# Optimization experiments

Hardware: AMD Instinct MI355X
Metric: run time of the kernel (lower is better)

The kernel has to match this reference:

```python
import jax, jax.numpy as jnp
import numpy as np

DIM = 768
HEADS = 12
HEAD_DIM = DIM // HEADS
SCALE = HEAD_DIM ** -0.5
EPS = 1e-6


def setup_inputs() -> dict:
    key = jax.random.key(0)
    ks = jax.random.split(key, 10)
    B, Nq, Nk, C = 4, 4096, 4096, DIM
    std = C ** -0.5
    return {
        "x_q": jax.random.normal(ks[0], (B, Nq, C), jnp.float32),
        "x_kv": jax.random.normal(ks[1], (B, Nk, C), jnp.float32),
        "Wq": jax.random.normal(ks[2], (C, C), jnp.float32) * std,
        "bq": jnp.zeros((C,), jnp.float32),
        "Wk": jax.random.normal(ks[3], (C, C), jnp.float32) * std,
        "bk": jnp.zeros((C,), jnp.float32),
        "Wv": jax.random.normal(ks[4], (C, C), jnp.float32) * std,
        "bv": jnp.zeros((C,), jnp.float32),
        "Wp": jax.random.normal(ks[5], (C, C), jnp.float32) * std,
        "bp": jnp.zeros((C,), jnp.float32),
    }


def _phi(x):
    # ELU(alpha=1) + 1 positive feature map
    return jax.nn.elu(x) + 1.0


def reference(x_q, x_kv, Wq, bq, Wk, bk, Wv, bv, Wp, bp):
    B, Nq, C = x_q.shape
    Nk = x_kv.shape[1]
    h, d = HEADS, HEAD_DIM
    # projections (torch Linear: x @ W.T + b)
    q = x_q @ Wq.T + bq   # [B,Nq,C]
    k = x_kv @ Wk.T + bk  # [B,Nk,C]
    v = x_kv @ Wv.T + bv  # [B,Nk,C]
    # split heads -> [B,h,N,d]
    q = q.reshape(B, Nq, h, d).transpose(0, 2, 1, 3) * SCALE
    k = k.reshape(B, Nk, h, d).transpose(0, 2, 1, 3)
    v = v.reshape(B, Nk, h, d).transpose(0, 2, 1, 3)
    q_phi = _phi(q)
    k_phi = _phi(k)
    # KV state [B,h,d,d] and normalizer sum [B,h,d]
    kv = jnp.einsum('bhnd,bhne->bhde', k_phi, v)
    k_sum = k_phi.sum(axis=2)
    out = jnp.einsum('bhnd,bhde->bhne', q_phi, kv)
    z = jnp.einsum('bhnd,bhd->bhn', q_phi, k_sum)[..., None] + EPS
    out = out / z
    out = out.transpose(0, 2, 1, 3).reshape(B, Nq, C)
    return out @ Wp.T + bp
```

## Files before the change

### kernel.cpp

```cpp
#include <hip/hip_runtime.h>
#include <hip/hip_bf16.h>
#include <cstdint>
#include <cstddef>

#define HD_B   4
#define SEQ    4096
#define CDIM   768
#define HEADS  12
#define HDIM   64
#define MROWS  (HD_B * SEQ)
#define QSCALE 0.125f
#define EPSV   1e-6f

typedef __attribute__((ext_vector_type(8))) short  short8v;
typedef __attribute__((ext_vector_type(4))) float  f32x4;

__device__ __forceinline__ unsigned short f2b(float f) {
    unsigned int u = __float_as_uint(f);
    u += 0x7FFFu + ((u >> 16) & 1u);
    return (unsigned short)(u >> 16);
}
__device__ __forceinline__ float b2f(unsigned short b) {
    return __uint_as_float(((unsigned int)b) << 16);
}
__device__ __forceinline__ float phi_f(float x) {
    return x > 0.f ? x + 1.f : __expf(x);
}

#define GLOAD_LDS16(g, l)                                             \
    __builtin_amdgcn_global_load_lds(                                 \
        (__attribute__((address_space(1))) void*)(void*)(g),          \
        (__attribute__((address_space(3))) void*)(l), 16, 0, 0)

#define VMW12() asm volatile("s_waitcnt vmcnt(12)" ::: "memory")
#define VMW8()  asm volatile("s_waitcnt vmcnt(8)"  ::: "memory")
#define VMW4()  asm volatile("s_waitcnt vmcnt(4)"  ::: "memory")
#define VMW0()  asm volatile("s_waitcnt vmcnt(0)"  ::: "memory")
#define LGW()   asm volatile("s_waitcnt lgkmcnt(0)" ::: "memory")
#define SB()    do { __builtin_amdgcn_sched_barrier(0);               \
                     __builtin_amdgcn_s_barrier();                    \
                     __builtin_amdgcn_sched_barrier(0); } while (0)

__global__ void wcvt_all(const float* __restrict__ wq, const float* __restrict__ wk,
                         const float* __restrict__ wv, const float* __restrict__ wp,
                         unsigned short* __restrict__ dst) {
    const int y = blockIdx.y;
    const float* src = (y == 0) ? wq : (y == 1) ? wk : (y == 2) ? wv : wp;
    const int i = blockIdx.x * 256 + threadIdx.x;
    float4 v = reinterpret_cast<const float4*>(src)[i];
    ushort4 o;
    o.x = f2b(v.x); o.y = f2b(v.y); o.z = f2b(v.z); o.w = f2b(v.w);
    reinterpret_cast<ushort4*>(dst + (size_t)y * (CDIM * CDIM))[i] = o;
}

template <int EPI, int NC>
__device__ __forceinline__ void proj_body(
    const float* __restrict__ A32,
    const unsigned short* __restrict__ Bp,
    const float* __restrict__ b0, const float* __restrict__ b1,
    unsigned short* __restrict__ o0, unsigned short* __restrict__ o1)
{
    constexpr int K  = CDIM;
    constexpr int T  = NC * 128;
    constexpr int NT = K / 64;

    __shared__ __align__(16) char smem[49152];
    char* As = smem;

    const int tid  = threadIdx.x;
    const int lane = tid & 63;
    const int w    = tid >> 6;
    const int wr   = w >> 1, wc = w & 1;

    const int bid  = blockIdx.x;
    const int s    = (bid & 7) * (T >> 3) + (bid >> 3);
    const int colp = s % NC;
    const int rowp = s / NC;
    const int brow = rowp * 128;
    const int bcol = colp * 128;

    const int r8  = lane >> 3;
    const int c8e = ((lane & 7) ^ r8) << 3;
    const int ar  = lane >> 4;
    const int ac  = (lane & 15) << 2;
    const int fr  = lane & 15;
    const int hi4 = lane >> 4;

    f32x4 acc[4][4];
#pragma unroll
    for (int i = 0; i < 4; ++i)
#pragma unroll
        for (int j = 0; j < 4; ++j)
            acc[i][j] = (f32x4){0.f, 0.f, 0.f, 0.f};

    auto stageB = [&](int buf, int kt) {
        char* dst = smem + 16384 + buf * 16384;
#pragma unroll
        for (int g = 0; g < 4; ++g) {
            const unsigned short* src =
                Bp + (size_t)(bcol + w * 32 + g * 8 + r8) * K + kt * 64 + c8e;
            GLOAD_LDS16(src, dst + (w * 32 + g * 8) * 128);
        }
    };

    float4 fA[8];
    auto aload = [&](int kt) {
#pragma unroll
        for (int j = 0; j < 8; ++j)
            fA[j] = *(const float4*)(A32 + (size_t)(brow + w * 32 + j * 4 + ar) * K
                                     + kt * 64 + ac);
    };
    auto awrite = [&]() {
#pragma unroll
        for (int j = 0; j < 8; ++j) {
            const int row = w * 32 + j * 4 + ar;
            unsigned int p0, p1;
            asm("v_cvt_pk_bf16_f32 %0, %1, %2" : "=v"(p0) : "v"(fA[j].x), "v"(fA[j].y));
            asm("v_cvt_pk_bf16_f32 %0, %1, %2" : "=v"(p1) : "v"(fA[j].z), "v"(fA[j].w));
            uint2 pk; pk.x = p0; pk.y = p1;
            *(uint2*)(As + row * 128 + ((ac << 1) ^ ((row & 7) << 4))) = pk;
        }
    };
    auto compute = [&](int bbuf) {
        const char* Bb = smem + 16384 + bbuf * 16384;
        short8v a[4][2];
#pragma unroll
        for (int i = 0; i < 4; ++i) {
            const int row = wr * 64 + i * 16 + fr;
#pragma unroll
            for (int ks = 0; ks < 2; ++ks)
                a[i][ks] = *(const short8v*)(As + row * 128 +
                              ((((ks << 2) + hi4) ^ (row & 7)) << 4));
        }
#pragma unroll
        for (int j = 0; j < 4; ++j) {
            const int row = wc * 64 + j * 16 + fr;
            short8v bb0 = *(const short8v*)(Bb + row * 128 + ((hi4 ^ (row & 7)) << 4));
            short8v bb1 = *(const short8v*)(Bb + row * 128 + (((4 + hi4) ^ (row & 7)) << 4));
#pragma unroll
            for (int i = 0; i < 4; ++i) {
                acc[i][j] = __builtin_amdgcn_mfma_f32_16x16x32_bf16(a[i][0], bb0, acc[i][j], 0, 0, 0);
                acc[i][j] = __builtin_amdgcn_mfma_f32_16x16x32_bf16(a[i][1], bb1, acc[i][j], 0, 0, 0);
            }
        }
    };

    aload(0);
    stageB(0, 0);
    VMW4();
    awrite();
    aload(1);
    stageB(1, 1);
    LGW();
    SB();

    for (int t = 0; t < NT; ++t) {
        const int c = t & 1;
        if (t == NT - 1) { VMW0(); } else { VMW12(); }
        SB();
        compute(c);
        SB();
        if (t < NT - 1) {
            VMW4();
            awrite();
            if (t < NT - 2) { aload(t + 2); stageB(c, t + 2); }
            LGW();
        }
    }

    float* ep = (float*)(void*)smem + w * (16 * 68);
    const int rr = lane >> 2;
    const int cb = (lane & 3) * 4;
    const bool isV = (EPI == 1) && (colp >= 6);
    const float* bptr = (EPI == 0) ? (b0 + bcol)
                        : (isV ? (b1 + (bcol - 768)) : (b0 + bcol));
    const int colbase = ((EPI == 1 && isV) ? bcol - 768 : bcol) + wc * 64;
    unsigned short* o16 = (EPI == 1 && isV) ? o1 : o0;

    float4 bb[4];
#pragma unroll
    for (int q = 0; q < 4; ++q)
        bb[q] = *(const float4*)&bptr[wc * 64 + q * 16 + cb];

#pragma unroll
    for (int i = 0; i < 4; ++i) {
#pragma unroll
        for (int j = 0; j < 4; ++j)
#pragma unroll
            for (int r = 0; r < 4; ++r)
                ep[(hi4 * 4 + r) * 68 + j * 16 + fr] = acc[i][j][r];
#pragma unroll
        for (int q = 0; q < 4; ++q) {
            const int cc = q * 16 + cb;
            f32x4 v = *(const f32x4*)&ep[rr * 68 + cc];
            const int rg = brow + wr * 64 + i * 16 + rr;
            const float4 bq = bb[q];
            ushort4 ov;
            if (EPI == 0) {
                ov.x = f2b(phi_f((v[0] + bq.x) * QSCALE));
                ov.y = f2b(phi_f((v[1] + bq.y) * QSCALE));
                ov.z = f2b(phi_f((v[2] + bq.z) * QSCALE));
                ov.w = f2b(phi_f((v[3] + bq.w) * QSCALE));
            } else if (!isV) {
                ov.x = f2b(phi_f(v[0] + bq.x));
                ov.y = f2b(phi_f(v[1] + bq.y));
                ov.z = f2b(phi_f(v[2] + bq.z));
                ov.w = f2b(phi_f(v[3] + bq.w));
            } else {
                ov.x = f2b(v[0] + bq.x);
                ov.y = f2b(v[1] + bq.y);
                ov.z = f2b(v[2] + bq.z);
                ov.w = f2b(v[3] + bq.w);
            }
            *(ushort4*)(o16 + (size_t)rg * 768 + (colbase + cc)) = ov;
        }
    }
}

__global__ __launch_bounds__(256, 3) void g_q(
    const float* __restrict__ xq, const unsigned short* __restrict__ wq,
    const float* __restrict__ bq, unsigned short* __restrict__ qphi)
{
    proj_body<0, 6>(xq, wq, bq, nullptr, qphi, nullptr);
}

__global__ __launch_bounds__(256, 3) void g_kv(
    const float* __restrict__ xkv, const unsigned short* __restrict__ wkv,
    const float* __restrict__ bk, const float* __restrict__ bv,
    unsigned short* __restrict__ kphi, unsigned short* __restrict__ v16)
{
    proj_body<1, 12>(xkv, wkv, bk, bv, kphi, v16);
}

__global__ __launch_bounds__(256) void g_out(
    const unsigned short* __restrict__ A16,
    const unsigned short* __restrict__ Bp,
    const float* __restrict__ bias,
    float* __restrict__ outp)
{
    constexpr int K  = CDIM;
    constexpr int NT = K / 64;
    __shared__ __align__(16) char smem[65536];

    const int tid  = threadIdx.x;
    const int lane = tid & 63;
    const int w    = tid >> 6;
    const int wr   = w >> 1, wc = w & 1;

    const int bid  = blockIdx.x;
    const int s    = (bid & 7) * (768 >> 3) + (bid >> 3);
    const int colp = s % 6;
    const int rowp = s / 6;
    const int brow = rowp * 128;
    const int bcol = colp * 128;

    const int r8  = lane >> 3;
    const int c8e = ((lane & 7) ^ r8) << 3;
    const int fr  = lane & 15;
    const int hi4 = lane >> 4;

    f32x4 acc[4][4];
#pragma unroll
    for (int i = 0; i < 4; ++i)
#pragma unroll
        for (int j = 0; j < 4; ++j)
            acc[i][j] = (f32x4){0.f, 0.f, 0.f, 0.f};

    auto stageA = [&](int buf, int kt) {
        char* dst = smem + buf * 16384;
#pragma unroll
        for (int g = 0; g < 4; ++g) {
            const unsigned short* src =
                A16 + (size_t)(brow + w * 32 + g * 8 + r8) * K + kt * 64 + c8e;
            GLOAD_LDS16(src, dst + (w * 32 + g * 8) * 128);
        }
    };
    auto stageB = [&](int buf, int kt) {
        char* dst = smem + 32768 + buf * 16384;
#pragma unroll
        for (int g = 0; g < 4; ++g) {
            const unsigned short* src =
                Bp + (size_t)(bcol + w * 32 + g * 8 + r8) * K + kt * 64 + c8e;
            GLOAD_LDS16(src, dst + (w * 32 + g * 8) * 128);
        }
    };
    auto compute = [&](int buf) {
        const char* Ab = smem + buf * 16384;
        const char* Bb = smem + 32768 + buf * 16384;
        short8v a[4][2], b[4][2];
#pragma unroll
        for (int i = 0; i < 4; ++i) {
            const int row = wr * 64 + i * 16 + fr;
#pragma unroll
            for (int ks = 0; ks < 2; ++ks)
                a[i][ks] = *(const short8v*)(Ab + row * 128 +
                              ((((ks << 2) + hi4) ^ (row & 7)) << 4));
        }
#pragma unroll
        for (int j = 0; j < 4; ++j) {
            const int row = wc * 64 + j * 16 + fr;
#pragma unroll
            for (int ks = 0; ks < 2; ++ks)
                b[j][ks] = *(const short8v*)(Bb + row * 128 +
                              ((((ks << 2) + hi4) ^ (row & 7)) << 4));
        }
#pragma unroll
        for (int i = 0; i < 4; ++i)
#pragma unroll
            for (int j = 0; j < 4; ++j) {
                acc[i][j] = __builtin_amdgcn_mfma_f32_16x16x32_bf16(a[i][0], b[j][0], acc[i][j], 0, 0, 0);
                acc[i][j] = __builtin_amdgcn_mfma_f32_16x16x32_bf16(a[i][1], b[j][1], acc[i][j], 0, 0, 0);
            }
    };

    stageA(0, 0); stageB(0, 0);
    stageA(1, 1); stageB(1, 1);
    for (int t = 0; t < NT; ++t) {
        const int c = t & 1;
        if (t == NT - 1) { VMW0(); } else { VMW8(); }
        SB();
        compute(c);
        SB();
        if (t < NT - 2) { stageA(c, t + 2); stageB(c, t + 2); }
    }

    float* ep = (float*)(void*)smem + w * (16 * 68);
    const int rr = lane >> 2;
    const int cb = (lane & 3) * 4;
    float4 bb[4];
#pragma unroll
    for (int q = 0; q < 4; ++q)
        bb[q] = *(const float4*)&bias[bcol + wc * 64 + q * 16 + cb];
#pragma unroll
    for (int i = 0; i < 4; ++i) {
#pragma unroll
        for (int j = 0; j < 4; ++j)
#pragma unroll
            for (int r = 0; r < 4; ++r)
                ep[(hi4 * 4 + r) * 68 + j * 16 + fr] = acc[i][j][r];
#pragma unroll
        for (int q = 0; q < 4; ++q) {
            const int cc = q * 16 + cb;
            f32x4 v = *(const f32x4*)&ep[rr * 68 + cc];
            const int rg = brow + wr * 64 + i * 16 + rr;
            const int cg = bcol + wc * 64 + cc;
            const float4 bq = bb[q];
            float4 ov;
            ov.x = v[0] + bq.x; ov.y = v[1] + bq.y;
            ov.z = v[2] + bq.z; ov.w = v[3] + bq.w;
            *(float4*)(outp + (size_t)rg * 768 + cg) = ov;
        }
    }
}

#define KVCH   128
#define KVITER 2
#define NCHUNK 16

__global__ __launch_bounds__(256, 3) void kv_part(
    const unsigned short* __restrict__ kphi,
    const unsigned short* __restrict__ vmat,
    float* __restrict__ part)
{
    const int bh = blockIdx.y;
    const int b  = bh / HEADS, h = bh % HEADS;
    const int c  = blockIdx.x;
    __shared__ unsigned short Kl[KVCH][HDIM];
    __shared__ float Vl[KVCH][HDIM];
    const int t  = threadIdx.x;
    const int i  = t >> 2;
    const int jb = t & 3;

    float acc[16];
#pragma unroll
    for (int jj = 0; jj < 16; ++jj) acc[jj] = 0.f;
    float ksum = 0.f;

    for (int it = 0; it < KVITER; ++it) {
        const size_t rbase = (size_t)b * SEQ + (size_t)c * (KVCH * KVITER) + it * KVCH;
        __syncthreads();
        for (int l = 0; l < KVCH / 32; ++l) {
            int row = l * 32 + (t >> 3);
            int col = (t & 7) << 3;
            const size_t g = (rbase + row) * CDIM + h * HDIM + col;
            int4 kk = *(const int4*)(kphi + g);
            int4 vv = *(const int4*)(vmat + g);
            *(int4*)&Kl[row][col] = kk;
            const unsigned short* vp = (const unsigned short*)&vv;
            float4 lo, hi;
            lo.x = b2f(vp[0]); lo.y = b2f(vp[1]); lo.z = b2f(vp[2]); lo.w = b2f(vp[3]);
            hi.x = b2f(vp[4]); hi.y = b2f(vp[5]); hi.z = b2f(vp[6]); hi.w = b2f(vp[7]);
            *(float4*)&Vl[row][col]     = lo;
            *(float4*)&Vl[row][col + 4] = hi;
        }
        __syncthreads();
        for (int n = 0; n < KVCH; ++n) {
            float kf = b2f(Kl[n][i]);
            const float4* vr = (const float4*)&Vl[n][jb * 16];
            float4 v0 = vr[0], v1 = vr[1], v2 = vr[2], v3 = vr[3];
            acc[0]  += kf * v0.x; acc[1]  += kf * v0.y; acc[2]  += kf * v0.z; acc[3]  += kf * v0.w;
            acc[4]  += kf * v1.x; acc[5]  += kf * v1.y; acc[6]  += kf * v1.z; acc[7]  += kf * v1.w;
            acc[8]  += kf * v2.x; acc[9]  += kf * v2.y; acc[10] += kf * v2.z; acc[11] += kf * v2.w;
            acc[12] += kf * v3.x; acc[13] += kf * v3.y; acc[14] += kf * v3.z; acc[15] += kf * v3.w;
            ksum += kf;
        }
    }
    float* op = part + ((size_t)c * 48 + bh) * 4160;
#pragma unroll
    for (int jj = 0; jj < 16; ++jj) op[i * 64 + jb * 16 + jj] = acc[jj];
    if (jb == 0) op[4096 + i] = ksum;
}

__global__ void kv_finalize(const float* __restrict__ part, float* __restrict__ kv) {
    int idx = blockIdx.x * 256 + threadIdx.x;
    if (idx >= 48 * 4160) return;
    float s = 0.f;
    for (int c = 0; c < NCHUNK; ++c) s += part[(size_t)c * 48 * 4160 + idx];
    kv[idx] = s;
}

__global__ __launch_bounds__(256) void attn_apply(
    const unsigned short* __restrict__ qphi,
    const float* __restrict__ kv,
    unsigned short* __restrict__ attn)
{
    const int h  = blockIdx.y;
    const int m0 = blockIdx.x * 64;
    const int b  = m0 >> 12;
    const int bh = b * HEADS + h;
    __shared__ float kvs[HDIM][HDIM];
    __shared__ float ksums[HDIM];
    __shared__ unsigned short ql[64][HDIM];
    const int t = threadIdx.x;
    const float* kvp = kv + (size_t)bh * 4160;
#pragma unroll
    for (int it = 0; it < 4; ++it) {
        int e = it * 1024 + t * 4;
        *(float4*)&kvs[e >> 6][e & 63] = *(const float4*)&kvp[e];
    }
    if (t < 64) ksums[t] = kvp[4096 + t];
#pragma unroll
    for (int it = 0; it < 2; ++it) {
        int row = it * 32 + (t >> 3);
        int col = (t & 7) << 3;
        *(int4*)&ql[row][col] =
            *(const int4*)(qphi + (size_t)(m0 + row) * CDIM + h * HDIM + col);
    }
    __syncthreads();

    const int r  = t >> 2;
    const int jb = t & 3;
    float acc[16];
#pragma unroll
    for (int jj = 0; jj < 16; ++jj) acc[jj] = 0.f;
    float z = 0.f;
    for (int q8 = 0; q8 < 8; ++q8) {
        short8v qv = *(const short8v*)&ql[r][q8 * 8];
#pragma unroll
        for (int dd = 0; dd < 8; ++dd) {
            float qd = b2f((unsigned short)qv[dd]);
            int d = q8 * 8 + dd;
            const float4* kr = (const float4*)&kvs[d][jb * 16];
            float4 k0 = kr[0], k1 = kr[1], k2 = kr[2], k3 = kr[3];
            acc[0]  += qd * k0.x; acc[1]  += qd * k0.y; acc[2]  += qd * k0.z; acc[3]  += qd * k0.w;
            acc[4]  += qd * k1.x; acc[5]  += qd * k1.y; acc[6]  += qd * k1.z; acc[7]  += qd * k1.w;
            acc[8]  += qd * k2.x; acc[9]  += qd * k2.y; acc[10] += qd * k2.z; acc[11] += qd * k2.w;
            acc[12] += qd * k3.x; acc[13] += qd * k3.y; acc[14] += qd * k3.z; acc[15] += qd * k3.w;
            z += qd * ksums[d];
        }
    }
    const float inv = 1.f / (z + EPSV);
    unsigned short* op = attn + (size_t)(m0 + r) * CDIM + h * HDIM + jb * 16;
#pragma unroll
    for (int jj = 0; jj < 16; ++jj) op[jj] = f2b(acc[jj] * inv);
}

extern "C" void kernel_launch(void* const* d_in, const int* in_sizes, int n_in,
                              void* d_out, int out_size, void* d_ws, size_t ws_size,
                              hipStream_t stream)
{
    const float* x_q  = (const float*)d_in[0];
    const float* x_kv = (const float*)d_in[1];
    const float* Wq   = (const float*)d_in[2];
    const float* bq   = (const float*)d_in[3];
    const float* Wk   = (const float*)d_in[4];
    const float* bk   = (const float*)d_in[5];
    const float* Wv   = (const float*)d_in[6];
    const float* bv   = (const float*)d_in[7];
    const float* Wp   = (const float*)d_in[8];
    const float* bp   = (const float*)d_in[9];
    float* out = (float*)d_out;

    char* ws = (char*)d_ws;
    size_t off = 0;
    auto alloc = [&](size_t bytes) -> char* {
        char* p = ws + off;
        off += (bytes + 255) & ~(size_t)255;
        return p;
    };
    const size_t xelems = (size_t)MROWS * CDIM;
    const size_t welems = (size_t)CDIM * CDIM;

    unsigned short* w16    = (unsigned short*)alloc(4 * welems * 2);
    unsigned short* wkv16  = w16 + welems;
    unsigned short* wp16   = w16 + 3 * welems;
    unsigned short* qphi   = (unsigned short*)alloc(xelems * 2);
    unsigned short* kphi   = (unsigned short*)alloc(xelems * 2);
    unsigned short* v16    = (unsigned short*)alloc(xelems * 2);
    unsigned short* attn16 = (unsigned short*)alloc(xelems * 2);
    float* part = (float*)alloc((size_t)NCHUNK * 48 * 4160 * 4);
    float* kvf  = (float*)alloc((size_t)48 * 4160 * 4);

    wcvt_all<<<dim3(576, 4), 256, 0, stream>>>(Wq, Wk, Wv, Wp, w16);

    g_q<<<768, 256, 0, stream>>>(x_q, w16, bq, qphi);

    g_kv<<<1536, 256, 0, stream>>>(x_kv, wkv16, bk, bv, kphi, v16);

    kv_part<<<dim3(NCHUNK, 48), 256, 0, stream>>>(kphi, v16, part);
    kv_finalize<<<(48 * 4160 + 255) / 256, 256, 0, stream>>>(part, kvf);
    attn_apply<<<dim3(MROWS / 64, HEADS), 256, 0, stream>>>(qphi, kvf, attn16);

    g_out<<<768, 256, 0, stream>>>(attn16, wp16, bp, out);
}
```

Baseline: 201.2 us.

## Use 8 waves per block in projection GEMMs with 64x32 per-wave tiles

Measured after the change: 450.3 us. 124% more time.

```diff
diff --git a/kernel.cpp b/kernel.cpp
--- a/kernel.cpp
+++ b/kernel.cpp
@@ -32,9 +32,9 @@
         (__attribute__((address_space(1))) void*)(void*)(g),          \
         (__attribute__((address_space(3))) void*)(l), 16, 0, 0)
 
-#define VMW12() asm volatile("s_waitcnt vmcnt(12)" ::: "memory")
-#define VMW8()  asm volatile("s_waitcnt vmcnt(8)"  ::: "memory")
+#define VMW6()  asm volatile("s_waitcnt vmcnt(6)"  ::: "memory")
 #define VMW4()  asm volatile("s_waitcnt vmcnt(4)"  ::: "memory")
+#define VMW2()  asm volatile("s_waitcnt vmcnt(2)"  ::: "memory")
 #define VMW0()  asm volatile("s_waitcnt vmcnt(0)"  ::: "memory")
 #define LGW()   asm volatile("s_waitcnt lgkmcnt(0)" ::: "memory")
 #define SB()    do { __builtin_amdgcn_sched_barrier(0);               \
@@ -54,7 +54,7 @@
 }
 
 template <int EPI, int NC>
-__device__ __forceinline__ void proj_body(
+__device__ __forceinline__ void proj_body8(
     const float* __restrict__ A32,
     const unsigned short* __restrict__ Bp,
     const float* __restrict__ b0, const float* __restrict__ b1,
@@ -70,7 +70,8 @@
     const int tid  = threadIdx.x;
     const int lane = tid & 63;
     const int w    = tid >> 6;
-    const int wr   = w >> 1, wc = w & 1;
+    const int wm   = w >> 2;
+    const int wn   = w & 3;
 
     const int bid  = blockIdx.x;
     const int s    = (bid & 7) * (T >> 3) + (bid >> 3);
@@ -86,34 +87,34 @@
     const int fr  = lane & 15;
     const int hi4 = lane >> 4;
 
-    f32x4 acc[4][4];
+    f32x4 acc[4][2];
 #pragma unroll
     for (int i = 0; i < 4; ++i)
 #pragma unroll
-        for (int j = 0; j < 4; ++j)
+        for (int j = 0; j < 2; ++j)
             acc[i][j] = (f32x4){0.f, 0.f, 0.f, 0.f};
 
     auto stageB = [&](int buf, int kt) {
         char* dst = smem + 16384 + buf * 16384;
 #pragma unroll
-        for (int g = 0; g < 4; ++g) {
+        for (int g = 0; g < 2; ++g) {
             const unsigned short* src =
-                Bp + (size_t)(bcol + w * 32 + g * 8 + r8) * K + kt * 64 + c8e;
-            GLOAD_LDS16(src, dst + (w * 32 + g * 8) * 128);
-        }
-    };
-
-    float4 fA[8];
+                Bp + (size_t)(bcol + w * 16 + g * 8 + r8) * K + kt * 64 + c8e;
+            GLOAD_LDS16(src, dst + (w * 16 + g * 8) * 128);
+        }
+    };
+
+    float4 fA[4];
     auto aload = [&](int kt) {
 #pragma unroll
-        for (int j = 0; j < 8; ++j)
-            fA[j] = *(const float4*)(A32 + (size_t)(brow + w * 32 + j * 4 + ar) * K
+        for (int j = 0; j < 4; ++j)
+            fA[j] = *(const float4*)(A32 + (size_t)(brow + w * 16 + j * 4 + ar) * K
                                      + kt * 64 + ac);
     };
     auto awrite = [&]() {
 #pragma unroll
-        for (int j = 0; j < 8; ++j) {
-            const int row = w * 32 + j * 4 + ar;
+        for (int j = 0; j < 4; ++j) {
+            const int row = w * 16 + j * 4 + ar;
             unsigned int p0, p1;
             asm("v_cvt_pk_bf16_f32 %0, %1, %2" : "=v"(p0) : "v"(fA[j].x), "v"(fA[j].y));
             asm("v_cvt_pk_bf16_f32 %0, %1, %2" : "=v"(p1) : "v"(fA[j].z), "v"(fA[j].w));
@@ -126,15 +127,15 @@
         short8v a[4][2];
 #pragma unroll
         for (int i = 0; i < 4; ++i) {
-            const int row = wr * 64 + i * 16 + fr;
+            const int row = wm * 64 + i * 16 + fr;
 #pragma unroll
             for (int ks = 0; ks < 2; ++ks)
                 a[i][ks] = *(const short8v*)(As + row * 128 +
                               ((((ks << 2) + hi4) ^ (row & 7)) << 4));
         }
 #pragma unroll
-        for (int j = 0; j < 4; ++j) {
-            const int row = wc * 64 + j * 16 + fr;
+        for (int j = 0; j < 2; ++j) {
+            const int row = wn * 32 + j * 16 + fr;
             short8v bb0 = *(const short8v*)(Bb + row * 128 + ((hi4 ^ (row & 7)) << 4));
             short8v bb1 = *(const short8v*)(Bb + row * 128 + (((4 + hi4) ^ (row & 7)) << 4));
 #pragma unroll
@@ -147,7 +148,7 @@
 
     aload(0);
     stageB(0, 0);
-    VMW4();
+    VMW2();
     awrite();
     aload(1);
     stageB(1, 1);
@@ -156,83 +157,70 @@
 
     for (int t = 0; t < NT; ++t) {
         const int c = t & 1;
-        if (t == NT - 1) { VMW0(); } else { VMW12(); }
+        if (t == NT - 1) { VMW0(); } else { VMW6(); }
         SB();
         compute(c);
         SB();
         if (t < NT - 1) {
-            VMW4();
+            VMW2();
             awrite();
             if (t < NT - 2) { aload(t + 2); stageB(c, t + 2); }
             LGW();
         }
     }
 
-    float* ep = (float*)(void*)smem + w * (16 * 68);
+    float* ep = (float*)(void*)smem + w * (16 * 36);
     const int rr = lane >> 2;
-    const int cb = (lane & 3) * 4;
+    const int cq = (lane & 3) * 8;
     const bool isV = (EPI == 1) && (colp >= 6);
     const float* bptr = (EPI == 0) ? (b0 + bcol)
                         : (isV ? (b1 + (bcol - 768)) : (b0 + bcol));
-    const int colbase = ((EPI == 1 && isV) ? bcol - 768 : bcol) + wc * 64;
+    const int colbase = ((EPI == 1 && isV) ? bcol - 768 : bcol) + wn * 32;
     unsigned short* o16 = (EPI == 1 && isV) ? o1 : o0;
 
-    float4 bb[4];
-#pragma unroll
-    for (int q = 0; q < 4; ++q)
-        bb[q] = *(const float4*)&bptr[wc * 64 + q * 16 + cb];
+    float4 bb0 = *(const float4*)&bptr[wn * 32 + cq];
+    float4 bb1 = *(const float4*)&bptr[wn * 32 + cq + 4];
 
 #pragma unroll
     for (int i = 0; i < 4; ++i) {
 #pragma unroll
-        for (int j = 0; j < 4; ++j)
+        for (int j = 0; j < 2; ++j)
 #pragma unroll
             for (int r = 0; r < 4; ++r)
-                ep[(hi4 * 4 + r) * 68 + j * 16 + fr] = acc[i][j][r];
-#pragma unroll
-        for (int q = 0; q < 4; ++q) {
-            const int cc = q * 16 + cb;
-            f32x4 v = *(const f32x4*)&ep[rr * 68 + cc];
-            const int rg = brow + wr * 64 + i * 16 + rr;
-            const float4 bq = bb[q];
-            ushort4 ov;
-            if (EPI == 0) {
-                ov.x = f2b(phi_f((v[0] + bq.x) * QSCALE));
-                ov.y = f2b(phi_f((v[1] + bq.y) * QSCALE));
-                ov.z = f2b(phi_f((v[2] + bq.z) * QSCALE));
-                ov.w = f2b(phi_f((v[3] + bq.w) * QSCALE));
-            } else if (!isV) {
-                ov.x = f2b(phi_f(v[0] + bq.x));
-                ov.y = f2b(phi_f(v[1] + bq.y));
-                ov.z = f2b(phi_f(v[2] + bq.z));
-                ov.w = f2b(phi_f(v[3] + bq.w));
-            } else {
-                ov.x = f2b(v[0] + bq.x);
-                ov.y = f2b(v[1] + bq.y);
-                ov.z = f2b(v[2] + bq.z);
-                ov.w = f2b(v[3] + bq.w);
-            }
-            *(ushort4*)(o16 + (size_t)rg * 768 + (colbase + cc)) = ov;
-        }
-    }
-}
-
-__global__ __launch_bounds__(256, 3) void g_q(
+                ep[(hi4 * 4 + r) * 36 + j * 16 + fr] = acc[i][j][r];
+        f32x4 v0 = *(const f32x4*)&ep[rr * 36 + cq];
+        f32x4 v1 = *(const f32x4*)&ep[rr * 36 + cq + 4];
+        const int rg = brow + wm * 64 + i * 16 + rr;
+        float o[8];
+        o[0] = v0[0] + bb0.x; o[1] = v0[1] + bb0.y; o[2] = v0[2] + bb0.z; o[3] = v0[3] + bb0.w;
+        o[4] = v1[0] + bb1.x; o[5] = v1[1] + bb1.y; o[6] = v1[2] + bb1.z; o[7] = v1[3] + bb1.w;
+        unsigned short ov[8];
+#pragma unroll
+        for (int e = 0; e < 8; ++e) {
+            if (EPI == 0)      ov[e] = f2b(phi_f(o[e] * QSCALE));
+            else if (!isV)     ov[e] = f2b(phi_f(o[e]));
+            else               ov[e] = f2b(o[e]);
+        }
+        *(int4*)(o16 + (size_t)rg * 768 + colbase + cq) = *(int4*)ov;
+    }
+}
+
+__global__ __launch_bounds__(512, 5) void g_q(
     const float* __restrict__ xq, const unsigned short* __restrict__ wq,
     const float* __restrict__ bq, unsigned short* __restrict__ qphi)
 {
-    proj_body<0, 6>(xq, wq, bq, nullptr, qphi, nullptr);
-}
-
-__global__ __launch_bounds__(256, 3) void g_kv(
+    proj_body8<0, 6>(xq, wq, bq, nullptr, qphi, nullptr);
+}
+
+__global__ __launch_bounds__(512, 5) void g_kv(
     const float* __restrict__ xkv, const unsigned short* __restrict__ wkv,
     const float* __restrict__ bk, const float* __restrict__ bv,
     unsigned short* __restrict__ kphi, unsigned short* __restrict__ v16)
 {
-    proj_body<1, 12>(xkv, wkv, bk, bv, kphi, v16);
-}
-
-__global__ __launch_bounds__(256) void g_out(
+    proj_body8<1, 12>(xkv, wkv, bk, bv, kphi, v16);
+}
+
+__global__ __launch_bounds__(512, 4) void g_out(
     const unsigned short* __restrict__ A16,
     const unsigned short* __restrict__ Bp,
     const float* __restrict__ bias,
@@ -245,7 +233,7 @@
     const int tid  = threadIdx.x;
     const int lane = tid & 63;
     const int w    = tid >> 6;
-    const int wr   = w >> 1, wc = w & 1;
+    const int wm   = w >> 2, wn = w & 3;
 
     const int bid  = blockIdx.x;
     const int s    = (bid & 7) * (768 >> 3) + (bid >> 3);
@@ -259,97 +247,83 @@
     const int fr  = lane & 15;
     const int hi4 = lane >> 4;
 
-    f32x4 acc[4][4];
+    f32x4 acc[4][2];
 #pragma unroll
     for (int i = 0; i < 4; ++i)
 #pragma unroll
-        for (int j = 0; j < 4; ++j)
+        for (int j = 0; j < 2; ++j)
             acc[i][j] = (f32x4){0.f, 0.f, 0.f, 0.f};
 
-    auto stageA = [&](int buf, int kt) {
-        char* dst = smem + buf * 16384;
-#pragma unroll
-        for (int g = 0; g < 4; ++g) {
-            const unsigned short* src =
-                A16 + (size_t)(brow + w * 32 + g * 8 + r8) * K + kt * 64 + c8e;
-            GLOAD_LDS16(src, dst + (w * 32 + g * 8) * 128);
-        }
-    };
-    auto stageB = [&](int buf, int kt) {
-        char* dst = smem + 32768 + buf * 16384;
-#pragma unroll
-        for (int g = 0; g < 4; ++g) {
-            const unsigned short* src =
-                Bp + (size_t)(bcol + w * 32 + g * 8 + r8) * K + kt * 64 + c8e;
-            GLOAD_LDS16(src, dst + (w * 32 + g * 8) * 128);
+    auto stage = [&](int buf, int kt) {
+        char* dstA = smem + buf * 16384;
+        char* dstB = smem + 32768 + buf * 16384;
+#pragma unroll
+        for (int g = 0; g < 2; ++g) {
+            const unsigned short* srcA =
+                A16 + (size_t)(brow + w * 16 + g * 8 + r8) * K + kt * 64 + c8e;
+            GLOAD_LDS16(srcA, dstA + (w * 16 + g * 8) * 128);
+            const unsigned short* srcB =
+                Bp + (size_t)(bcol + w * 16 + g * 8 + r8) * K + kt * 64 + c8e;
+            GLOAD_LDS16(srcB, dstB + (w * 16 + g * 8) * 128);
         }
     };
     auto compute = [&](int buf) {
         const char* Ab = smem + buf * 16384;
         const char* Bb = smem + 32768 + buf * 16384;
-        short8v a[4][2], b[4][2];
+        short8v a[4][2];
 #pragma unroll
         for (int i = 0; i < 4; ++i) {
-            const int row = wr * 64 + i * 16 + fr;
+            const int row = wm * 64 + i * 16 + fr;
 #pragma unroll
             for (int ks = 0; ks < 2; ++ks)
                 a[i][ks] = *(const short8v*)(Ab + row * 128 +
                               ((((ks << 2) + hi4) ^ (row & 7)) << 4));
         }
 #pragma unroll
-        for (int j = 0; j < 4; ++j) {
-            const int row = wc * 64 + j * 16 + fr;
-#pragma unroll
-            for (int ks = 0; ks < 2; ++ks)
-                b[j][ks] = *(const short8v*)(Bb + row * 128 +
-                              ((((ks << 2) + hi4) ^ (row & 7)) << 4));
-        }
-#pragma unroll
-        for (int i = 0; i < 4; ++i)
-#pragma unroll
-            for (int j = 0; j < 4; ++j) {
-                acc[i][j] = __builtin_amdgcn_mfma_f32_16x16x32_bf16(a[i][0], b[j][0], acc[i][j], 0, 0, 0);
-                acc[i][j] = __builtin_amdgcn_mfma_f32_16x16x32_bf16(a[i][1], b[j][1], acc[i][j], 0, 0, 0);
+        for (int j = 0; j < 2; ++j) {
+            const int row = wn * 32 + j * 16 + fr;
+            short8v bb0 = *(const short8v*)(Bb + row * 128 + ((hi4 ^ (row & 7)) << 4));
+            short8v bb1 = *(const short8v*)(Bb + row * 128 + (((4 + hi4) ^ (row & 7)) << 4));
+#pragma unroll
+            for (int i = 0; i < 4; ++i) {
+                acc[i][j] = __builtin_amdgcn_mfma_f32_16x16x32_bf16(a[i][0], bb0, acc[i][j], 0, 0, 0);
+                acc[i][j] = __builtin_amdgcn_mfma_f32_16x16x32_bf16(a[i][1], bb1, acc[i][j], 0, 0, 0);
             }
-    };
-
-    stageA(0, 0); stageB(0, 0);
-    stageA(1, 1); stageB(1, 1);
+        }
+    };
+
+    stage(0, 0);
+    stage(1, 1);
     for (int t = 0; t < NT; ++t) {
         const int c = t & 1;
-        if (t == NT - 1) { VMW0(); } else { VMW8(); }
+        if (t == NT - 1) { VMW0(); } else { VMW4(); }
         SB();
         compute(c);
         SB();
-        if (t < NT - 2) { stageA(c, t + 2); stageB(c, t + 2); }
-    }
-
-    float* ep = (float*)(void*)smem + w * (16 * 68);
+        if (t < NT - 2) stage(c, t + 2);
+    }
+
+    float* ep = (float*)(void*)smem + w * (16 * 36);
     const int rr = lane >> 2;
-    const int cb = (lane & 3) * 4;
-    float4 bb[4];
-#pragma unroll
-    for (int q = 0; q < 4; ++q)
-        bb[q] = *(const float4*)&bias[bcol + wc * 64 + q * 16 + cb];
+    const int cq = (lane & 3) * 8;
+    float4 bb0 = *(const float4*)&bias[bcol + wn * 32 + cq];
+    float4 bb1 = *(const float4*)&bias[bcol + wn * 32 + cq + 4];
 #pragma unroll
     for (int i = 0; i < 4; ++i) {
 #pragma unroll
-        for (int j = 0; j < 4; ++j)
+        for (int j = 0; j < 2; ++j)
 #pragma unroll
             for (int r = 0; r < 4; ++r)
-                ep[(hi4 * 4 + r) * 68 + j * 16 + fr] = acc[i][j][r];
-#pragma unroll
-        for (int q = 0; q < 4; ++q) {
-            const int cc = q * 16 + cb;
-            f32x4 v = *(const f32x4*)&ep[rr * 68 + cc];
-            const int rg = brow + wr * 64 + i * 16 + rr;
-            const int cg = bcol + wc * 64 + cc;
-            const float4 bq = bb[q];
-            float4 ov;
-            ov.x = v[0] + bq.x; ov.y = v[1] + bq.y;
-            ov.z = v[2] + bq.z; ov.w = v[3] + bq.w;
-            *(float4*)(outp + (size_t)rg * 768 + cg) = ov;
-        }
+                ep[(hi4 * 4 + r) * 36 + j * 16 + fr] = acc[i][j][r];
+        f32x4 v0 = *(const f32x4*)&ep[rr * 36 + cq];
+        f32x4 v1 = *(const f32x4*)&ep[rr * 36 + cq + 4];
+        const int rg = brow + wm * 64 + i * 16 + rr;
+        float* op = outp + (size_t)rg * 768 + bcol + wn * 32 + cq;
+        float4 s0, s1;
+        s0.x = v0[0] + bb0.x; s0.y = v0[1] + bb0.y; s0.z = v0[2] + bb0.z; s0.w = v0[3] + bb0.w;
+        s1.x = v1[0] + bb1.x; s1.y = v1[1] + bb1.y; s1.z = v1[2] + bb1.z; s1.w = v1[3] + bb1.w;
+        *(float4*)op = s0;
+        *(float4*)(op + 4) = s1;
     }
 }
 
@@ -513,13 +487,13 @@
 
     wcvt_all<<<dim3(576, 4), 256, 0, stream>>>(Wq, Wk, Wv, Wp, w16);
 
-    g_q<<<768, 256, 0, stream>>>(x_q, w16, bq, qphi);
-
-    g_kv<<<1536, 256, 0, stream>>>(x_kv, wkv16, bk, bv, kphi, v16);
+    g_q<<<768, 512, 0, stream>>>(x_q, w16, bq, qphi);
+
+    g_kv<<<1536, 512, 0, stream>>>(x_kv, wkv16, bk, bv, kphi, v16);
 
     kv_part<<<dim3(NCHUNK, 48), 256, 0, stream>>>(kphi, v16, part);
     kv_finalize<<<(48 * 4160 + 255) / 256, 256, 0, stream>>>(part, kvf);
     attn_apply<<<dim3(MROWS / 64, HEADS), 256, 0, stream>>>(qphi, kvf, attn16);
 
-    g_out<<<768, 256, 0, stream>>>(attn16, wp16, bp, out);
-}
+    g_out<<<768, 512, 0, stream>>>(attn16, wp16, bp, out);
+}
```

## Stage output-GEMM A tile through registers to cut LDS and raise occupancy

Applied to the files above, without the earlier changes.

Result: slower. 230.1 us (+14.4%).

```diff
diff --git a/kernel.cpp b/kernel.cpp
--- a/kernel.cpp
+++ b/kernel.cpp
@@ -232,7 +232,7 @@
     proj_body<1, 12>(xkv, wkv, bk, bv, kphi, v16);
 }
 
-__global__ __launch_bounds__(256) void g_out(
+__global__ __launch_bounds__(256, 3) void g_out(
     const unsigned short* __restrict__ A16,
     const unsigned short* __restrict__ Bp,
     const float* __restrict__ bias,
@@ -240,7 +240,8 @@
 {
     constexpr int K  = CDIM;
     constexpr int NT = K / 64;
-    __shared__ __align__(16) char smem[65536];
+    __shared__ __align__(16) char smem[49152];
+    char* As = smem;
 
     const int tid  = threadIdx.x;
     const int lane = tid & 63;
@@ -266,17 +267,8 @@
         for (int j = 0; j < 4; ++j)
             acc[i][j] = (f32x4){0.f, 0.f, 0.f, 0.f};
 
-    auto stageA = [&](int buf, int kt) {
-        char* dst = smem + buf * 16384;
-#pragma unroll
-        for (int g = 0; g < 4; ++g) {
-            const unsigned short* src =
-                A16 + (size_t)(brow + w * 32 + g * 8 + r8) * K + kt * 64 + c8e;
-            GLOAD_LDS16(src, dst + (w * 32 + g * 8) * 128);
-        }
-    };
     auto stageB = [&](int buf, int kt) {
-        char* dst = smem + 32768 + buf * 16384;
+        char* dst = smem + 16384 + buf * 16384;
 #pragma unroll
         for (int g = 0; g < 4; ++g) {
             const unsigned short* src =
@@ -284,44 +276,66 @@
             GLOAD_LDS16(src, dst + (w * 32 + g * 8) * 128);
         }
     };
-    auto compute = [&](int buf) {
-        const char* Ab = smem + buf * 16384;
-        const char* Bb = smem + 32768 + buf * 16384;
-        short8v a[4][2], b[4][2];
+
+    int4 rA[4];
+    auto aload = [&](int kt) {
+#pragma unroll
+        for (int g = 0; g < 4; ++g)
+            rA[g] = *(const int4*)(A16 + (size_t)(brow + w * 32 + g * 8 + r8) * K
+                                   + kt * 64 + ((lane & 7) << 3));
+    };
+    auto awrite = [&]() {
+#pragma unroll
+        for (int g = 0; g < 4; ++g) {
+            const int row = w * 32 + g * 8 + r8;
+            *(int4*)(As + row * 128 + (((lane & 7) ^ r8) << 4)) = rA[g];
+        }
+    };
+    auto compute = [&](int bbuf) {
+        const char* Bb = smem + 16384 + bbuf * 16384;
+        short8v a[4][2];
 #pragma unroll
         for (int i = 0; i < 4; ++i) {
             const int row = wr * 64 + i * 16 + fr;
 #pragma unroll
             for (int ks = 0; ks < 2; ++ks)
-                a[i][ks] = *(const short8v*)(Ab + row * 128 +
+                a[i][ks] = *(const short8v*)(As + row * 128 +
                               ((((ks << 2) + hi4) ^ (row & 7)) << 4));
         }
 #pragma unroll
         for (int j = 0; j < 4; ++j) {
             const int row = wc * 64 + j * 16 + fr;
-#pragma unroll
-            for (int ks = 0; ks < 2; ++ks)
-                b[j][ks] = *(const short8v*)(Bb + row * 128 +
-                              ((((ks << 2) + hi4) ^ (row & 7)) << 4));
-        }
-#pragma unroll
-        for (int i = 0; i < 4; ++i)
-#pragma unroll
-            for (int j = 0; j < 4; ++j) {
-                acc[i][j] = __builtin_amdgcn_mfma_f32_16x16x32_bf16(a[i][0], b[j][0], acc[i][j], 0, 0, 0);
-                acc[i][j] = __builtin_amdgcn_mfma_f32_16x16x32_bf16(a[i][1], b[j][1], acc[i][j], 0, 0, 0);
+            short8v bb0 = *(const short8v*)(Bb + row * 128 + ((hi4 ^ (row & 7)) << 4));
+            short8v bb1 = *(const short8v*)(Bb + row * 128 + (((4 + hi4) ^ (row & 7)) << 4));
+#pragma unroll
+            for (int i = 0; i < 4; ++i) {
+                acc[i][j] = __builtin_amdgcn_mfma_f32_16x16x32_bf16(a[i][0], bb0, acc[i][j], 0, 0, 0);
+                acc[i][j] = __builtin_amdgcn_mfma_f32_16x16x32_bf16(a[i][1], bb1, acc[i][j], 0, 0, 0);
             }
-    };
-
-    stageA(0, 0); stageB(0, 0);
-    stageA(1, 1); stageB(1, 1);
+        }
+    };
+
+    aload(0);
+    stageB(0, 0);
+    VMW4();
+    awrite();
+    aload(1);
+    stageB(1, 1);
+    LGW();
+    SB();
+
     for (int t = 0; t < NT; ++t) {
         const int c = t & 1;
         if (t == NT - 1) { VMW0(); } else { VMW8(); }
         SB();
         compute(c);
         SB();
-        if (t < NT - 2) { stageA(c, t + 2); stageB(c, t + 2); }
+        if (t < NT - 1) {
+            VMW4();
+            awrite();
+            if (t < NT - 2) { aload(t + 2); stageB(c, t + 2); }
+            LGW();
+        }
     }
 
     float* ep = (float*)(void*)smem + w * (16 * 68);
```
